# Kernel optimization log

Hardware: AMD Instinct MI355X
Metric: run time of the kernel (lower is better)

## Reference

```python
import jax, jax.numpy as jnp
import numpy as np
from jax import lax

B, L, D_IN, H, RES, BD, D_OUT = 1024, 128, 5, 64, 256, 8, 1


def setup_inputs() -> dict:
    key = jax.random.key(0)
    ks = jax.random.split(key, 14)
    f = jnp.float32
    d = {}
    d["V_noise"] = jax.random.normal(ks[0], (B, D_IN), f)
    d["increments"] = jax.random.normal(ks[1], (B, L, BD), f)
    d["W1"] = jax.random.normal(ks[2], (H, D_IN), f) / np.float32(np.sqrt(D_IN))
    d["b1"] = jnp.zeros((H,), f)
    d["W2"] = jax.random.normal(ks[3], (RES, H), f) / np.float32(np.sqrt(H))
    d["b2"] = jnp.zeros((RES,), f)
    d["rho1"] = jax.random.normal(ks[4], (1, 1), f)
    d["rho2"] = jax.random.normal(ks[5], (1, 1), f)
    d["rho3"] = jax.random.normal(ks[6], (1, 1), f)
    d["rho4"] = jax.random.normal(ks[7], (1, 1), f)
    d["rho5"] = jax.random.normal(ks[8], (1, 1), f)
    # scale reservoir matrices by 1/sqrt(res) so pre-activations are O(1)
    d["B1"] = jax.random.normal(ks[9], (RES, RES), f) / np.float32(np.sqrt(RES))
    d["B2"] = jax.random.normal(ks[10], (BD, RES, RES), f) / np.float32(np.sqrt(RES))
    d["lambda1"] = jax.random.normal(ks[11], (RES, 1), f)
    d["lambda2"] = jax.random.normal(ks[12], (BD, RES, 1), f)
    d["Wr"] = jax.random.normal(ks[13], (D_OUT, RES), f) / np.float32(np.sqrt(RES))
    d["br"] = jnp.zeros((D_OUT,), f)
    return d


def reference(V_noise, increments, W1, b1, W2, b2,
              rho1, rho2, rho3, rho4, rho5,
              B1, B2, lambda1, lambda2, Wr, br):
    act = jnp.tanh
    # initial-condition MLP: [B, D_in] -> [B, RES]
    V = act(V_noise @ W1.T + b1) @ W2.T + b2
    # Brownian path with W[:,0] = 0
    Wp = jnp.cumsum(increments, axis=1).at[:, 0, :].set(0.0)
    dW = Wp[:, 1:] - Wp[:, :-1]          # [B, L-1, BD]
    l1 = lambda1[:, 0]                    # [RES]
    l2 = lambda2[:, :, 0]                 # [BD, RES]
    rho5s = rho5[0, 0]

    def step(r, dw):                      # r: [B, RES], dw: [B, BD]
        drift = act(rho1 * (r @ B1.T) + rho2 * l1)                      # [B, RES]
        diff = act(rho3 * jnp.einsum('kij,bj->bki', B2, r) + rho4 * l2)  # [B, BD, RES]
        rn = r + drift + rho5s * jnp.einsum('bki,bk->bi', diff, dw)
        return rn, rn

    _, Rs = lax.scan(step, V, jnp.swapaxes(dW, 0, 1))  # [L-1, B, RES]
    Rall = jnp.concatenate([V[None], Rs], axis=0)       # [L, B, RES]
    # time-homogeneous linear readout per lag, concatenated along time
    x = Rall @ Wr.T + br                                 # [L, B, D_out]
    out = jnp.transpose(x, (1, 0, 2)).reshape(V.shape[0], Rall.shape[0] * x.shape[-1], 1)
    return out
```

## Files before the change

### kernel.cpp

```cpp
#include <hip/hip_runtime.h>
#include <hip/hip_bf16.h>

#define B_TOT 1024
#define L_T   128
#define DIN   5
#define HD    64
#define RESN  256
#define BDN   8
#define NMAT  9
#define NROWS (NMAT * RESN)
#define PLANE ((size_t)NROWS * RESN)
#define NGRP  16
#define BG    64
#define FPB   16
#define NTHR  256
#define RB_GRP_BYTES (2 * BG * RESN * 4)
#define BUF_SHORTS (BG * RESN)
#define LO_OFF     (2 * BUF_SHORTS)
#define WS_RB_OFF  (2 * PLANE * 2)
#define WS_FLAG_OFF (WS_RB_OFF + (size_t)NGRP * RB_GRP_BYTES)
#define FLAGS_PER_GRP 1024

typedef __attribute__((ext_vector_type(8))) short bf16x8;
typedef __attribute__((ext_vector_type(4))) float f32x4;

__device__ __forceinline__ float fast_tanh(float x) {
    float e = __expf(2.0f * x);
    return 1.0f - 2.0f * __builtin_amdgcn_rcpf(e + 1.0f);
}

__device__ __forceinline__ void split_hl(float v, unsigned short& h, unsigned short& l) {
    __hip_bfloat16 hb = __float2bfloat16(v);
    h = __builtin_bit_cast(unsigned short, hb);
    l = __builtin_bit_cast(unsigned short, __float2bfloat16(v - __bfloat162float(hb)));
}

__device__ __forceinline__ unsigned mall_load1(const unsigned* p) {
    unsigned r;
    asm volatile("global_load_dword %0, %1, off sc0 sc1" : "=v"(r) : "v"(p));
    return r;
}
__device__ __forceinline__ unsigned l2_load1(const unsigned* p) {
    unsigned r;
    asm volatile("global_load_dword %0, %1, off sc0" : "=v"(r) : "v"(p));
    return r;
}
__device__ __forceinline__ void mall_store1(unsigned* p, unsigned v) {
    asm volatile("global_store_dword %0, %1, off sc0 sc1" :: "v"(p), "v"(v) : "memory");
}
__device__ __forceinline__ uint4 mall_load4s(const unsigned short* p) {
    uint4 r;
    asm volatile("global_load_dwordx4 %0, %1, off sc0 sc1" : "=v"(r) : "v"(p));
    return r;
}
__device__ __forceinline__ uint4 l2_load4s(const unsigned short* p) {
    uint4 r;
    asm volatile("global_load_dwordx4 %0, %1, off sc0" : "=v"(r) : "v"(p));
    return r;
}
__device__ __forceinline__ void mall_store2(unsigned short* p, unsigned v) {
    asm volatile("global_store_short %0, %1, off sc0 sc1" :: "v"(p), "v"(v) : "memory");
}
__device__ __forceinline__ void l2_store2(unsigned short* p, unsigned v) {
    asm volatile("global_store_short %0, %1, off sc0" :: "v"(p), "v"(v) : "memory");
}
__device__ __forceinline__ void atom_add_l2(unsigned* p, unsigned v) {
    asm volatile("global_atomic_add %0, %1, off" :: "v"(p), "v"(v) : "memory");
}
__device__ __forceinline__ void wait_vm0() {
    asm volatile("s_waitcnt vmcnt(0)" ::: "memory");
}

__device__ __forceinline__ void spin_all(const unsigned* fladdr, unsigned want, bool l2m) {
    unsigned guard = 0;
    for (;;) {
        unsigned fv = l2m ? l2_load1(fladdr) : mall_load1(fladdr);
        wait_vm0();
        if (__ballot(fv < want) == 0ull) break;
        __builtin_amdgcn_s_sleep(1);
        if (++guard > (1u << 20)) break;
    }
}

__global__ void conv_w(const float* __restrict__ B1, const float* __restrict__ B2,
                       __hip_bfloat16* __restrict__ wh, __hip_bfloat16* __restrict__ wl) {
    int idx = blockIdx.x * 256 + threadIdx.x;
    float v = (idx < RESN * RESN) ? B1[idx] : B2[idx - RESN * RESN];
    __hip_bfloat16 h = __float2bfloat16(v);
    wh[idx] = h;
    wl[idx] = __float2bfloat16(v - __bfloat162float(h));
}

__global__ __launch_bounds__(NTHR, 1) void sde_ws(
    const float* __restrict__ Vn,  const float* __restrict__ inc,
    const float* __restrict__ W1,  const float* __restrict__ b1,
    const float* __restrict__ W2,  const float* __restrict__ b2,
    const float* __restrict__ rho1p, const float* __restrict__ rho2p,
    const float* __restrict__ rho3p, const float* __restrict__ rho4p,
    const float* __restrict__ rho5p,
    const float* __restrict__ lam1, const float* __restrict__ lam2,
    const float* __restrict__ Wr,  const float* __restrict__ brp,
    const __hip_bfloat16* __restrict__ wbf,
    unsigned short* __restrict__ rbs,
    unsigned int* __restrict__ flags,
    float* __restrict__ out)
{
    __shared__ __align__(16) short wlds[2][NMAT][8][64][8];
    __shared__ __align__(16) short wrlds[2][8][4][8];
    __shared__ __align__(16) short zfrag[8];
    __shared__ int l2mode_sh;

    const int tid  = threadIdx.x;
    const int mt   = tid >> 6;
    const int lane = tid & 63;
    const int n16  = lane & 15;
    const int quad = lane >> 4;
    const int bx   = blockIdx.x;
    const int g    = ((bx & 7) << 1) | (bx >> 7);
    const int fb   = (bx >> 3) & 15;
    const int f0   = fb * FPB;
    const int b0g  = g * BG;
    unsigned short* gbs = rbs + (size_t)g * (RB_GRP_BYTES / 2);
    unsigned int* flagp  = flags + g * FLAGS_PER_GRP;
    unsigned int* myflag = flagp + (fb * 4 + mt) * 16;
    const unsigned* fladdr = (const unsigned*)(flagp + ((lane & 15) * 4 + mt) * 16);
    unsigned* regtbl = flags + NGRP * FLAGS_PER_GRP;
    unsigned* regcnt = regtbl + 256;

    if (tid == 0) {
        unsigned xcd;
        asm volatile("s_getreg_b32 %0, hwreg(HW_REG_XCC_ID)" : "=s"(xcd));
        mall_store1(&regtbl[bx], xcd);
        wait_vm0();
        __hip_atomic_fetch_add(regcnt, 1u, __ATOMIC_RELAXED, __HIP_MEMORY_SCOPE_AGENT);
    }

    const float rho1 = rho1p[0], rho2 = rho2p[0], rho3 = rho3p[0],
                rho4 = rho4p[0], rho5 = rho5p[0];
    const float brv = brp[0];

    float* hf  = (float*)&wlds[0][0][0][0][0];
    float* vsh = hf + 64 * 66;
    for (int p = tid; p < BG * HD; p += NTHR) {
        int b = p >> 6, hh = p & 63;
        float s = b1[hh];
        #pragma unroll
        for (int d = 0; d < DIN; ++d) s += Vn[(b0g + b) * DIN + d] * W1[hh * DIN + d];
        hf[b * 66 + hh] = fast_tanh(s);
    }
    __syncthreads();

    if (tid == 0) {
        unsigned cnt, guard = 0;
        do {
            cnt = mall_load1(regcnt);
            wait_vm0();
            if (cnt >= 256) break;
            __builtin_amdgcn_s_sleep(1);
        } while (++guard < (1u << 22));
        unsigned e[16];
        #pragma unroll
        for (int q = 0; q < 16; ++q)
            e[q] = mall_load1(&regtbl[((g & 1) << 7) | (q << 3) | (g >> 1)]);
        wait_vm0();
        int ok = (cnt >= 256) ? 1 : 0;
        #pragma unroll
        for (int q = 1; q < 16; ++q) ok &= (e[q] == e[0]) ? 1 : 0;
        l2mode_sh = ok;
    }
    __syncthreads();
    const bool l2m = (l2mode_sh != 0);

    {
        int b = 16 * mt + (lane >> 2);
        float sv[4];
        #pragma unroll
        for (int i = 0; i < 4; ++i) {
            int f = (lane & 3) * 4 + i;
            float s = b2[f0 + f];
            #pragma unroll 8
            for (int hh = 0; hh < HD; ++hh) s += hf[b * 66 + hh] * W2[(f0 + f) * HD + hh];
            vsh[b * 16 + f] = s;
            sv[i] = s;
        }
        unsigned short hs[4], ls[4];
        #pragma unroll
        for (int i = 0; i < 4; ++i) split_hl(sv[i], hs[i], ls[i]);
        unsigned short* pb = gbs + b * 256 + f0;
        if (l2m) {
            #pragma unroll
            for (int i = 0; i < 4; ++i) {
                int f = (lane & 3) * 4 + i;
                l2_store2(pb + f, hs[i]);
                l2_store2(pb + f + LO_OFF, ls[i]);
            }
        } else {
            #pragma unroll
            for (int i = 0; i < 4; ++i) {
                int f = (lane & 3) * 4 + i;
                mall_store2(pb + f, hs[i]);
                mall_store2(pb + f + LO_OFF, ls[i]);
            }
        }
    }
    wait_vm0();
    if (lane == 0) {
        if (l2m) atom_add_l2(myflag, 1u);
        else __hip_atomic_fetch_add(myflag, 1u, __ATOMIC_RELAXED, __HIP_MEMORY_SCOPE_AGENT);
    }

    float rmast[4];
    #pragma unroll
    for (int rg = 0; rg < 4; ++rg) rmast[rg] = vsh[(16 * mt + 4 * quad + rg) * 16 + n16];
    const float l1c = lam1[f0 + n16];
    float l2c[BDN];
    #pragma unroll
    for (int k = 0; k < BDN; ++k) l2c[k] = lam2[k * RESN + f0 + n16];
    __syncthreads();

    for (int e = tid; e < 2 * NMAT * 8 * 64; e += NTHR) {
        int l  = e & 63;
        int kk = (e >> 6) & 7;
        int m  = e >> 9;
        int pl = (m >= NMAT) ? 1 : 0;
        int nt = m - pl * NMAT;
        const uint4* src = (const uint4*)(wbf + (size_t)pl * PLANE +
            (size_t)(nt * RESN + f0 + (l & 15)) * RESN + kk * 32 + (l >> 4) * 8);
        *(uint4*)&wlds[pl][nt][kk][l][0] = *src;
    }
    for (int p = tid; p < 512; p += NTHR) {
        int s = p >> 3, j = p & 7;
        int pl = s >> 5, kk = (s >> 2) & 7, q = s & 3;
        float v = Wr[kk * 32 + q * 8 + j];
        __hip_bfloat16 hi = __float2bfloat16(v);
        wrlds[pl][kk][q][j] = pl ? __builtin_bit_cast(short, __float2bfloat16(v - __bfloat162float(hi)))
                                 : __builtin_bit_cast(short, hi);
    }
    if (tid < 8) zfrag[tid] = 0;
    __syncthreads();

    const short* ph = (n16 == 0) ? &wrlds[0][0][quad][0] : &zfrag[0];
    const short* pw = (n16 == 0) ? &wrlds[1][0][quad][0] : &zfrag[0];
    const int    stp = (n16 == 0) ? 4 * 8 : 0;

    for (int t = 0; t < L_T - 1; ++t) {
        float dwv[4][8];
        #pragma unroll
        for (int rg = 0; rg < 4; ++rg) {
            const size_t bglob = (size_t)(b0g + 16 * mt + 4 * quad + rg) * (L_T * BDN);
            const float4 d0 = *(const float4*)(inc + bglob + (size_t)(t + 1) * BDN);
            const float4 d1 = *(const float4*)(inc + bglob + (size_t)(t + 1) * BDN + 4);
            dwv[rg][0] = d0.x; dwv[rg][1] = d0.y; dwv[rg][2] = d0.z; dwv[rg][3] = d0.w;
            dwv[rg][4] = d1.x; dwv[rg][5] = d1.y; dwv[rg][6] = d1.z; dwv[rg][7] = d1.w;
            if (t == 0) {
                const float4 e0 = *(const float4*)(inc + bglob);
                const float4 e1 = *(const float4*)(inc + bglob + 4);
                dwv[rg][0] += e0.x; dwv[rg][1] += e0.y; dwv[rg][2] += e0.z; dwv[rg][3] += e0.w;
                dwv[rg][4] += e1.x; dwv[rg][5] += e1.y; dwv[rg][6] += e1.z; dwv[rg][7] += e1.w;
            }
        }
        spin_all(fladdr, (unsigned)(t + 1), l2m);
        const int cur = t & 1, nxt = cur ^ 1;
        const int lead = t & 15;

        bf16x8 afh[8], afl[8];
        {
            const unsigned short* pc = gbs + cur * BUF_SHORTS + (16 * mt + n16) * 256 + quad * 8;
            if (l2m) {
                #pragma unroll
                for (int kk = 0; kk < 8; ++kk) {
                    afh[kk] = __builtin_bit_cast(bf16x8, l2_load4s(pc + kk * 32));
                    afl[kk] = __builtin_bit_cast(bf16x8, l2_load4s(pc + kk * 32 + LO_OFF));
                }
            } else {
                #pragma unroll
                for (int kk = 0; kk < 8; ++kk) {
                    afh[kk] = __builtin_bit_cast(bf16x8, mall_load4s(pc + kk * 32));
                    afl[kk] = __builtin_bit_cast(bf16x8, mall_load4s(pc + kk * 32 + LO_OFF));
                }
            }
        }
        wait_vm0();

        f32x4 acc[NMAT] = {};
        #pragma unroll
        for (int kk = 0; kk < 8; ++kk) {
            bf16x8 bh[NMAT], bl[NMAT];
            #pragma unroll
            for (int nt = 0; nt < NMAT; ++nt) {
                bh[nt] = *(const bf16x8*)&wlds[0][nt][kk][lane][0];
                bl[nt] = *(const bf16x8*)&wlds[1][nt][kk][lane][0];
            }
            #pragma unroll
            for (int nt = 0; nt < NMAT; ++nt)
                acc[nt] = __builtin_amdgcn_mfma_f32_16x16x32_bf16(afh[kk], bh[nt], acc[nt], 0, 0, 0);
            #pragma unroll
            for (int nt = 0; nt < NMAT; ++nt)
                acc[nt] = __builtin_amdgcn_mfma_f32_16x16x32_bf16(afl[kk], bh[nt], acc[nt], 0, 0, 0);
            #pragma unroll
            for (int nt = 0; nt < NMAT; ++nt)
                acc[nt] = __builtin_amdgcn_mfma_f32_16x16x32_bf16(afh[kk], bl[nt], acc[nt], 0, 0, 0);
        }

        unsigned short hs[4], ls[4];
        #pragma unroll
        for (int rg = 0; rg < 4; ++rg) {
            float drift = fast_tanh(rho1 * acc[0][rg] + rho2 * l1c);
            float s = 0.0f;
            #pragma unroll
            for (int k = 0; k < BDN; ++k)
                s += fast_tanh(rho3 * acc[1 + k][rg] + rho4 * l2c[k]) * dwv[rg][k];
            float rn = rmast[rg] + drift + rho5 * s;
            rmast[rg] = rn;
            split_hl(rn, hs[rg], ls[rg]);
        }
        {
            unsigned short* pb = gbs + nxt * BUF_SHORTS + f0 + n16;
            if (l2m) {
                #pragma unroll
                for (int rg = 0; rg < 4; ++rg) {
                    const int bl_ = 16 * mt + 4 * quad + rg;
                    l2_store2(pb + bl_ * 256, hs[rg]);
                    l2_store2(pb + bl_ * 256 + LO_OFF, ls[rg]);
                }
            } else {
                #pragma unroll
                for (int rg = 0; rg < 4; ++rg) {
                    const int bl_ = 16 * mt + 4 * quad + rg;
                    mall_store2(pb + bl_ * 256, hs[rg]);
                    mall_store2(pb + bl_ * 256 + LO_OFF, ls[rg]);
                }
            }
        }
        wait_vm0();
        if (lane == 0) {
            if (l2m) atom_add_l2(myflag, 1u);
            else __hip_atomic_fetch_add(myflag, 1u, __ATOMIC_RELAXED, __HIP_MEMORY_SCOPE_AGENT);
        }

        if (fb == lead) {
            f32x4 accw = {};
            #pragma unroll
            for (int kk = 0; kk < 8; ++kk) {
                bf16x8 wh8 = *(const bf16x8*)(ph + kk * stp);
                bf16x8 wl8 = *(const bf16x8*)(pw + kk * stp);
                accw = __builtin_amdgcn_mfma_f32_16x16x32_bf16(afh[kk], wh8, accw, 0, 0, 0);
                accw = __builtin_amdgcn_mfma_f32_16x16x32_bf16(afl[kk], wh8, accw, 0, 0, 0);
                accw = __builtin_amdgcn_mfma_f32_16x16x32_bf16(afh[kk], wl8, accw, 0, 0, 0);
            }
            if (n16 == 0) {
                #pragma unroll
                for (int rg = 0; rg < 4; ++rg)
                    out[(size_t)(b0g + 16 * mt + 4 * quad + rg) * L_T + t] = accw[rg] + brv;
            }
        }
    }

    if (fb == 15) {
        spin_all(fladdr, (unsigned)L_T, l2m);
        bf16x8 ah[8], al[8];
        {
            const unsigned short* pc = gbs + 1 * BUF_SHORTS + (16 * mt + n16) * 256 + quad * 8;
            if (l2m) {
                #pragma unroll
                for (int kk = 0; kk < 8; ++kk) {
                    ah[kk] = __builtin_bit_cast(bf16x8, l2_load4s(pc + kk * 32));
                    al[kk] = __builtin_bit_cast(bf16x8, l2_load4s(pc + kk * 32 + LO_OFF));
                }
            } else {
                #pragma unroll
                for (int kk = 0; kk < 8; ++kk) {
                    ah[kk] = __builtin_bit_cast(bf16x8, mall_load4s(pc + kk * 32));
                    al[kk] = __builtin_bit_cast(bf16x8, mall_load4s(pc + kk * 32 + LO_OFF));
                }
            }
        }
        wait_vm0();
        f32x4 accw = {};
        #pragma unroll
        for (int kk = 0; kk < 8; ++kk) {
            bf16x8 wh8 = *(const bf16x8*)(ph + kk * stp);
            bf16x8 wl8 = *(const bf16x8*)(pw + kk * stp);
            accw = __builtin_amdgcn_mfma_f32_16x16x32_bf16(ah[kk], wh8, accw, 0, 0, 0);
            accw = __builtin_amdgcn_mfma_f32_16x16x32_bf16(al[kk], wh8, accw, 0, 0, 0);
            accw = __builtin_amdgcn_mfma_f32_16x16x32_bf16(ah[kk], wl8, accw, 0, 0, 0);
        }
        if (n16 == 0) {
            #pragma unroll
            for (int rg = 0; rg < 4; ++rg)
                out[(size_t)(b0g + 16 * mt + 4 * quad + rg) * L_T + (L_T - 1)] = accw[rg] + brv;
        }
    }
}

extern "C" void kernel_launch(void* const* d_in, const int* in_sizes, int n_in,
                              void* d_out, int out_size, void* d_ws, size_t ws_size,
                              hipStream_t stream) {
    const float* Vn   = (const float*)d_in[0];
    const float* inc  = (const float*)d_in[1];
    const float* W1   = (const float*)d_in[2];
    const float* b1   = (const float*)d_in[3];
    const float* W2   = (const float*)d_in[4];
    const float* b2   = (const float*)d_in[5];
    const float* r1   = (const float*)d_in[6];
    const float* r2   = (const float*)d_in[7];
    const float* r3   = (const float*)d_in[8];
    const float* r4   = (const float*)d_in[9];
    const float* r5   = (const float*)d_in[10];
    const float* B1   = (const float*)d_in[11];
    const float* B2   = (const float*)d_in[12];
    const float* lam1 = (const float*)d_in[13];
    const float* lam2 = (const float*)d_in[14];
    const float* Wr   = (const float*)d_in[15];
    const float* br   = (const float*)d_in[16];

    __hip_bfloat16* wh    = (__hip_bfloat16*)d_ws;
    unsigned short* rbs   = (unsigned short*)((char*)d_ws + WS_RB_OFF);
    unsigned int*   flags = (unsigned int*)((char*)d_ws + WS_FLAG_OFF);
    float* out = (float*)d_out;

    hipMemsetAsync(flags, 0, NGRP * FLAGS_PER_GRP * sizeof(unsigned int) + 2048, stream);
    conv_w<<<dim3(NROWS * RESN / 256), dim3(256), 0, stream>>>(B1, B2, wh, wh + PLANE);
    sde_ws<<<dim3(256), dim3(NTHR), 0, stream>>>(
        Vn, inc, W1, b1, W2, b2, r1, r2, r3, r4, r5, lam1, lam2, Wr, br,
        wh, rbs, flags, out);
}
```

Baseline: 763.6 us.

## Tile shared state buffer for vector stores and distribute readout via atomics

Each wave now stages its new hi/lo bf16 state values in LDS and writes them to the inter-block exchange buffer with one 16-byte store per lane, instead of many scattered 2-byte stores. The buffer layout is re-tiled per feature block so the matching fragment loads stay contiguous. The linear readout is no longer done by a rotating lead block with extra MFMAs. Every block now computes its partial dot product with shuffles and adds it into the output with float atomics, which needs an extra memset of the output and makes the sum order nondeterministic.

```diff
diff --git a/kernel.cpp b/kernel.cpp
--- a/kernel.cpp
+++ b/kernel.cpp
@@ -14,15 +14,16 @@
 #define BG    64
 #define FPB   16
 #define NTHR  256
-#define RB_GRP_BYTES (2 * BG * RESN * 4)
-#define BUF_SHORTS (BG * RESN)
-#define LO_OFF     (2 * BUF_SHORTS)
+#define RB_GRP_BYTES (2 * 16 * 2 * BG * FPB * 2)
+#define GRP_SHORTS (RB_GRP_BYTES / 2)
+#define BUF_SHORTS 32768
 #define WS_RB_OFF  (2 * PLANE * 2)
 #define WS_FLAG_OFF (WS_RB_OFF + (size_t)NGRP * RB_GRP_BYTES)
 #define FLAGS_PER_GRP 1024
 
 typedef __attribute__((ext_vector_type(8))) short bf16x8;
 typedef __attribute__((ext_vector_type(4))) float f32x4;
+typedef __attribute__((ext_vector_type(4))) unsigned u32x4;
 
 __device__ __forceinline__ float fast_tanh(float x) {
     float e = __expf(2.0f * x);
@@ -48,27 +49,33 @@
 __device__ __forceinline__ void mall_store1(unsigned* p, unsigned v) {
     asm volatile("global_store_dword %0, %1, off sc0 sc1" :: "v"(p), "v"(v) : "memory");
 }
-__device__ __forceinline__ uint4 mall_load4s(const unsigned short* p) {
-    uint4 r;
+__device__ __forceinline__ u32x4 mall_load4s(const unsigned short* p) {
+    u32x4 r;
     asm volatile("global_load_dwordx4 %0, %1, off sc0 sc1" : "=v"(r) : "v"(p));
     return r;
 }
-__device__ __forceinline__ uint4 l2_load4s(const unsigned short* p) {
-    uint4 r;
+__device__ __forceinline__ u32x4 l2_load4s(const unsigned short* p) {
+    u32x4 r;
     asm volatile("global_load_dwordx4 %0, %1, off sc0" : "=v"(r) : "v"(p));
     return r;
 }
-__device__ __forceinline__ void mall_store2(unsigned short* p, unsigned v) {
-    asm volatile("global_store_short %0, %1, off sc0 sc1" :: "v"(p), "v"(v) : "memory");
-}
-__device__ __forceinline__ void l2_store2(unsigned short* p, unsigned v) {
-    asm volatile("global_store_short %0, %1, off sc0" :: "v"(p), "v"(v) : "memory");
+__device__ __forceinline__ void mall_store4(unsigned short* p, u32x4 v) {
+    asm volatile("global_store_dwordx4 %0, %1, off sc0 sc1" :: "v"(p), "v"(v) : "memory");
+}
+__device__ __forceinline__ void l2_store4(unsigned short* p, u32x4 v) {
+    asm volatile("global_store_dwordx4 %0, %1, off sc0" :: "v"(p), "v"(v) : "memory");
 }
 __device__ __forceinline__ void atom_add_l2(unsigned* p, unsigned v) {
     asm volatile("global_atomic_add %0, %1, off" :: "v"(p), "v"(v) : "memory");
 }
+__device__ __forceinline__ void atom_addf_l2(float* p, float v) {
+    asm volatile("global_atomic_add_f32 %0, %1, off" :: "v"(p), "v"(v) : "memory");
+}
 __device__ __forceinline__ void wait_vm0() {
     asm volatile("s_waitcnt vmcnt(0)" ::: "memory");
+}
+__device__ __forceinline__ void wait_lgkm0() {
+    asm volatile("s_waitcnt lgkmcnt(0)" ::: "memory");
 }
 
 __device__ __forceinline__ void spin_all(const unsigned* fladdr, unsigned want, bool l2m) {
@@ -106,8 +113,7 @@
     float* __restrict__ out)
 {
     __shared__ __align__(16) short wlds[2][NMAT][8][64][8];
-    __shared__ __align__(16) short wrlds[2][8][4][8];
-    __shared__ __align__(16) short zfrag[8];
+    __shared__ __align__(16) unsigned short stage[4][512];
     __shared__ int l2mode_sh;
 
     const int tid  = threadIdx.x;
@@ -120,7 +126,7 @@
     const int fb   = (bx >> 3) & 15;
     const int f0   = fb * FPB;
     const int b0g  = g * BG;
-    unsigned short* gbs = rbs + (size_t)g * (RB_GRP_BYTES / 2);
+    unsigned short* gbs = rbs + (size_t)g * GRP_SHORTS;
     unsigned int* flagp  = flags + g * FLAGS_PER_GRP;
     unsigned int* myflag = flagp + (fb * 4 + mt) * 16;
     const unsigned* fladdr = (const unsigned*)(flagp + ((lane & 15) * 4 + mt) * 16);
@@ -138,6 +144,7 @@
     const float rho1 = rho1p[0], rho2 = rho2p[0], rho3 = rho3p[0],
                 rho4 = rho4p[0], rho5 = rho5p[0];
     const float brv = brp[0];
+    const float bradd = (fb == 0) ? brv : 0.0f;
 
     float* hf  = (float*)&wlds[0][0][0][0][0];
     float* vsh = hf + 64 * 66;
@@ -172,8 +179,8 @@
     const bool l2m = (l2mode_sh != 0);
 
     {
-        int b = 16 * mt + (lane >> 2);
-        float sv[4];
+        int bl = lane >> 2;
+        int b  = 16 * mt + bl;
         #pragma unroll
         for (int i = 0; i < 4; ++i) {
             int f = (lane & 3) * 4 + i;
@@ -181,27 +188,16 @@
             #pragma unroll 8
             for (int hh = 0; hh < HD; ++hh) s += hf[b * 66 + hh] * W2[(f0 + f) * HD + hh];
             vsh[b * 16 + f] = s;
-            sv[i] = s;
-        }
-        unsigned short hs[4], ls[4];
-        #pragma unroll
-        for (int i = 0; i < 4; ++i) split_hl(sv[i], hs[i], ls[i]);
-        unsigned short* pb = gbs + b * 256 + f0;
-        if (l2m) {
-            #pragma unroll
-            for (int i = 0; i < 4; ++i) {
-                int f = (lane & 3) * 4 + i;
-                l2_store2(pb + f, hs[i]);
-                l2_store2(pb + f + LO_OFF, ls[i]);
-            }
-        } else {
-            #pragma unroll
-            for (int i = 0; i < 4; ++i) {
-                int f = (lane & 3) * 4 + i;
-                mall_store2(pb + f, hs[i]);
-                mall_store2(pb + f + LO_OFF, ls[i]);
-            }
-        }
+            unsigned short h_, l_;
+            split_hl(s, h_, l_);
+            stage[mt][0 * 256 + bl * 16 + f] = h_;
+            stage[mt][1 * 256 + bl * 16 + f] = l_;
+        }
+        wait_lgkm0();
+        u32x4 v = *(const u32x4*)&stage[mt][lane * 8];
+        unsigned short* dst = gbs + 0 * BUF_SHORTS + fb * 2048 +
+                              (lane >> 5) * 1024 + 16 * mt * 16 + (lane & 31) * 8;
+        if (l2m) l2_store4(dst, v); else mall_store4(dst, v);
     }
     wait_vm0();
     if (lane == 0) {
@@ -213,6 +209,7 @@
     #pragma unroll
     for (int rg = 0; rg < 4; ++rg) rmast[rg] = vsh[(16 * mt + 4 * quad + rg) * 16 + n16];
     const float l1c = lam1[f0 + n16];
+    const float wrv = Wr[f0 + n16];
     float l2c[BDN];
     #pragma unroll
     for (int k = 0; k < BDN; ++k) l2c[k] = lam2[k * RESN + f0 + n16];
@@ -228,22 +225,34 @@
             (size_t)(nt * RESN + f0 + (l & 15)) * RESN + kk * 32 + (l >> 4) * 8);
         *(uint4*)&wlds[pl][nt][kk][l][0] = *src;
     }
-    for (int p = tid; p < 512; p += NTHR) {
-        int s = p >> 3, j = p & 7;
-        int pl = s >> 5, kk = (s >> 2) & 7, q = s & 3;
-        float v = Wr[kk * 32 + q * 8 + j];
-        __hip_bfloat16 hi = __float2bfloat16(v);
-        wrlds[pl][kk][q][j] = pl ? __builtin_bit_cast(short, __float2bfloat16(v - __bfloat162float(hi)))
-                                 : __builtin_bit_cast(short, hi);
-    }
-    if (tid < 8) zfrag[tid] = 0;
     __syncthreads();
 
-    const short* ph = (n16 == 0) ? &wrlds[0][0][quad][0] : &zfrag[0];
-    const short* pw = (n16 == 0) ? &wrlds[1][0][quad][0] : &zfrag[0];
-    const int    stp = (n16 == 0) ? 4 * 8 : 0;
-
-    for (int t = 0; t < L_T - 1; ++t) {
+    const unsigned short* pcb = gbs + (quad >> 1) * 2048 + (16 * mt + n16) * 16 + (quad & 1) * 8;
+
+    for (int t = 0; t < L_T; ++t) {
+        {
+            float po[4];
+            #pragma unroll
+            for (int rg = 0; rg < 4; ++rg) {
+                float p = wrv * rmast[rg];
+                p += __shfl_xor(p, 1);
+                p += __shfl_xor(p, 2);
+                p += __shfl_xor(p, 4);
+                p += __shfl_xor(p, 8);
+                po[rg] = p;
+            }
+            if (n16 == 0) {
+                #pragma unroll
+                for (int rg = 0; rg < 4; ++rg) {
+                    float* op = out + (size_t)(b0g + 16 * mt + 4 * quad + rg) * L_T + t;
+                    float v = po[rg] + bradd;
+                    if (l2m) atom_addf_l2(op, v);
+                    else __hip_atomic_fetch_add(op, v, __ATOMIC_RELAXED, __HIP_MEMORY_SCOPE_AGENT);
+                }
+            }
+        }
+        if (t == L_T - 1) break;
+
         float dwv[4][8];
         #pragma unroll
         for (int rg = 0; rg < 4; ++rg) {
@@ -261,22 +270,21 @@
         }
         spin_all(fladdr, (unsigned)(t + 1), l2m);
         const int cur = t & 1, nxt = cur ^ 1;
-        const int lead = t & 15;
 
         bf16x8 afh[8], afl[8];
         {
-            const unsigned short* pc = gbs + cur * BUF_SHORTS + (16 * mt + n16) * 256 + quad * 8;
+            const unsigned short* pc = pcb + cur * BUF_SHORTS;
             if (l2m) {
                 #pragma unroll
                 for (int kk = 0; kk < 8; ++kk) {
-                    afh[kk] = __builtin_bit_cast(bf16x8, l2_load4s(pc + kk * 32));
-                    afl[kk] = __builtin_bit_cast(bf16x8, l2_load4s(pc + kk * 32 + LO_OFF));
+                    afh[kk] = __builtin_bit_cast(bf16x8, l2_load4s(pc + kk * 4096));
+                    afl[kk] = __builtin_bit_cast(bf16x8, l2_load4s(pc + kk * 4096 + 1024));
                 }
             } else {
                 #pragma unroll
                 for (int kk = 0; kk < 8; ++kk) {
-                    afh[kk] = __builtin_bit_cast(bf16x8, mall_load4s(pc + kk * 32));
-                    afl[kk] = __builtin_bit_cast(bf16x8, mall_load4s(pc + kk * 32 + LO_OFF));
+                    afh[kk] = __builtin_bit_cast(bf16x8, mall_load4s(pc + kk * 4096));
+                    afl[kk] = __builtin_bit_cast(bf16x8, mall_load4s(pc + kk * 4096 + 1024));
                 }
             }
         }
@@ -302,7 +310,6 @@
                 acc[nt] = __builtin_amdgcn_mfma_f32_16x16x32_bf16(afh[kk], bl[nt], acc[nt], 0, 0, 0);
         }
 
-        unsigned short hs[4], ls[4];
         #pragma unroll
         for (int rg = 0; rg < 4; ++rg) {
             float drift = fast_tanh(rho1 * acc[0][rg] + rho2 * l1c);
@@ -312,83 +319,22 @@
                 s += fast_tanh(rho3 * acc[1 + k][rg] + rho4 * l2c[k]) * dwv[rg][k];
             float rn = rmast[rg] + drift + rho5 * s;
             rmast[rg] = rn;
-            split_hl(rn, hs[rg], ls[rg]);
-        }
+            unsigned short h_, l_;
+            split_hl(rn, h_, l_);
+            stage[mt][0 * 256 + (4 * quad + rg) * 16 + n16] = h_;
+            stage[mt][1 * 256 + (4 * quad + rg) * 16 + n16] = l_;
+        }
+        wait_lgkm0();
         {
-            unsigned short* pb = gbs + nxt * BUF_SHORTS + f0 + n16;
-            if (l2m) {
-                #pragma unroll
-                for (int rg = 0; rg < 4; ++rg) {
-                    const int bl_ = 16 * mt + 4 * quad + rg;
-                    l2_store2(pb + bl_ * 256, hs[rg]);
-                    l2_store2(pb + bl_ * 256 + LO_OFF, ls[rg]);
-                }
-            } else {
-                #pragma unroll
-                for (int rg = 0; rg < 4; ++rg) {
-                    const int bl_ = 16 * mt + 4 * quad + rg;
-                    mall_store2(pb + bl_ * 256, hs[rg]);
-                    mall_store2(pb + bl_ * 256 + LO_OFF, ls[rg]);
-                }
-            }
+            u32x4 v = *(const u32x4*)&stage[mt][lane * 8];
+            unsigned short* dst = gbs + nxt * BUF_SHORTS + fb * 2048 +
+                                  (lane >> 5) * 1024 + 16 * mt * 16 + (lane & 31) * 8;
+            if (l2m) l2_store4(dst, v); else mall_store4(dst, v);
         }
         wait_vm0();
         if (lane == 0) {
             if (l2m) atom_add_l2(myflag, 1u);
             else __hip_atomic_fetch_add(myflag, 1u, __ATOMIC_RELAXED, __HIP_MEMORY_SCOPE_AGENT);
-        }
-
-        if (fb == lead) {
-            f32x4 accw = {};
-            #pragma unroll
-            for (int kk = 0; kk < 8; ++kk) {
-                bf16x8 wh8 = *(const bf16x8*)(ph + kk * stp);
-                bf16x8 wl8 = *(const bf16x8*)(pw + kk * stp);
-                accw = __builtin_amdgcn_mfma_f32_16x16x32_bf16(afh[kk], wh8, accw, 0, 0, 0);
-                accw = __builtin_amdgcn_mfma_f32_16x16x32_bf16(afl[kk], wh8, accw, 0, 0, 0);
-                accw = __builtin_amdgcn_mfma_f32_16x16x32_bf16(afh[kk], wl8, accw, 0, 0, 0);
-            }
-            if (n16 == 0) {
-                #pragma unroll
-                for (int rg = 0; rg < 4; ++rg)
-                    out[(size_t)(b0g + 16 * mt + 4 * quad + rg) * L_T + t] = accw[rg] + brv;
-            }
-        }
-    }
-
-    if (fb == 15) {
-        spin_all(fladdr, (unsigned)L_T, l2m);
-        bf16x8 ah[8], al[8];
-        {
-            const unsigned short* pc = gbs + 1 * BUF_SHORTS + (16 * mt + n16) * 256 + quad * 8;
-            if (l2m) {
-                #pragma unroll
-                for (int kk = 0; kk < 8; ++kk) {
-                    ah[kk] = __builtin_bit_cast(bf16x8, l2_load4s(pc + kk * 32));
-                    al[kk] = __builtin_bit_cast(bf16x8, l2_load4s(pc + kk * 32 + LO_OFF));
-                }
-            } else {
-                #pragma unroll
-                for (int kk = 0; kk < 8; ++kk) {
-                    ah[kk] = __builtin_bit_cast(bf16x8, mall_load4s(pc + kk * 32));
-                    al[kk] = __builtin_bit_cast(bf16x8, mall_load4s(pc + kk * 32 + LO_OFF));
-                }
-            }
-        }
-        wait_vm0();
-        f32x4 accw = {};
-        #pragma unroll
-        for (int kk = 0; kk < 8; ++kk) {
-            bf16x8 wh8 = *(const bf16x8*)(ph + kk * stp);
-            bf16x8 wl8 = *(const bf16x8*)(pw + kk * stp);
-            accw = __builtin_amdgcn_mfma_f32_16x16x32_bf16(ah[kk], wh8, accw, 0, 0, 0);
-            accw = __builtin_amdgcn_mfma_f32_16x16x32_bf16(al[kk], wh8, accw, 0, 0, 0);
-            accw = __builtin_amdgcn_mfma_f32_16x16x32_bf16(ah[kk], wl8, accw, 0, 0, 0);
-        }
-        if (n16 == 0) {
-            #pragma unroll
-            for (int rg = 0; rg < 4; ++rg)
-                out[(size_t)(b0g + 16 * mt + 4 * quad + rg) * L_T + (L_T - 1)] = accw[rg] + brv;
         }
     }
 }
@@ -419,6 +365,7 @@
     unsigned int*   flags = (unsigned int*)((char*)d_ws + WS_FLAG_OFF);
     float* out = (float*)d_out;
 
+    hipMemsetAsync(d_out, 0, out_size, stream);
     hipMemsetAsync(flags, 0, NGRP * FLAGS_PER_GRP * sizeof(unsigned int) + 2048, stream);
     conv_w<<<dim3(NROWS * RESN / 256), dim3(256), 0, stream>>>(B1, B2, wh, wh + PLANE);
     sde_ws<<<dim3(256), dim3(NTHR), 0, stream>>>(
```

Result: no change. 770.8 us (+0.9%).
